# Kernel tuning notes

Hardware: AMD Instinct MI355X
Metric: run time of the kernel (lower is better)

Reference implementation:

```python
import jax, jax.numpy as jnp
import numpy as np

L, D = 6, 2048


def setup_inputs() -> dict:
    key = jax.random.key(0)
    ks = jax.random.split(key, 6)
    # 0.05 scale keeps repeated matrix compositions numerically tame
    W_upper = jax.random.normal(ks[0], (L, D, D), dtype=jnp.float32) * 0.05
    W_lower = jax.random.normal(ks[1], (L, D, D), dtype=jnp.float32) * 0.05
    b_upper = jax.random.normal(ks[2], (L, D), dtype=jnp.float32)
    b_lower = jax.random.normal(ks[3], (L, D), dtype=jnp.float32)
    ub = jax.random.normal(ks[4], (L, D), dtype=jnp.float32)
    lb = jax.random.normal(ks[5], (L, D), dtype=jnp.float32)
    return dict(W_upper=W_upper, W_lower=W_lower, b_upper=b_upper,
                b_lower=b_lower, ub=ub, lb=lb)


def _pos(W):
    # M * W  where M = (W >= 0)
    return jnp.where(W >= 0, W, jnp.zeros_like(W))


def _neg(W):
    # ~M * W where M = (W >= 0)
    return jnp.where(W >= 0, jnp.zeros_like(W), W)


def reference(W_upper, W_lower, b_upper, b_lower, ub, lb):
    # Layer index L-1 is `self`; backsubstitute toward layer 0 (input layer).
    Wu, Wl = W_upper[-1], W_lower[-1]          # [D, D]
    bu, bl = b_upper[-1], b_lower[-1]          # [D]
    best_ub, best_lb = ub[-1], lb[-1]          # [D]
    n_layers = W_upper.shape[0]
    for i in range(n_layers - 2, -1, -1):      # prev = layer i
        Wu_p, Wu_n = _pos(Wu), _neg(Wu)
        Wl_p, Wl_n = _pos(Wl), _neg(Wl)
        # concrete bounds through prev's pre-activation bounds
        cur_ub = Wu_p @ ub[i] + Wu_n @ lb[i] + bu
        cur_lb = Wl_p @ lb[i] + Wl_n @ ub[i] + bl
        best_ub = jnp.minimum(best_ub, cur_ub)
        best_lb = jnp.maximum(best_lb, cur_lb)
        # compose symbolic bounds with prev layer's relaxation
        bu = Wu_p @ b_upper[i] + Wu_n @ b_lower[i] + bu
        bl = Wl_p @ b_lower[i] + Wl_n @ b_upper[i] + bl
        Wu = Wu_p @ W_upper[i] + Wu_n @ W_lower[i]
        Wl = Wl_p @ W_lower[i] + Wl_n @ W_upper[i]
    # final concretization against the input layer's bounds (layer 0)
    Wu_p, Wu_n = _pos(Wu), _neg(Wu)
    Wl_p, Wl_n = _pos(Wl), _neg(Wl)
    cur_ub = Wu_p @ ub[0] + Wu_n @ lb[0] + bu
    cur_lb = Wl_p @ lb[0] + Wl_n @ ub[0] + bl
    best_ub = jnp.minimum(best_ub, cur_ub)
    best_lb = jnp.maximum(best_lb, cur_lb)
    return best_ub, best_lb
```

## Files before the change

kernel.cpp:

```cpp
#include <hip/hip_runtime.h>

#define D 2048
#define DD ((size_t)D * (size_t)D)

typedef __attribute__((ext_vector_type(8))) short bf16x8;
typedef __attribute__((ext_vector_type(16))) float f32x16;

#define GLOBAL_AS __attribute__((address_space(1)))
#define LDS_AS __attribute__((address_space(3)))

__device__ inline unsigned short f2bf(float f) {
  unsigned u = __float_as_uint(f);
  u += 0x7fffu + ((u >> 16) & 1u);
  return (unsigned short)(u >> 16);
}

__global__ void init_vecs(const float* __restrict__ b_upper5,
                          const float* __restrict__ b_lower5,
                          const float* __restrict__ ub5,
                          const float* __restrict__ lb5,
                          float* __restrict__ bu, float* __restrict__ bl,
                          float* __restrict__ out) {
  int t = blockIdx.x * blockDim.x + threadIdx.x;
  if (t < D) {
    bu[t] = b_upper5[t];
    bl[t] = b_lower5[t];
    out[t] = ub5[t];
    out[D + t] = lb5[t];
  }
}

__global__ __launch_bounds__(256) void prep(
    const float* __restrict__ Wu, const float* __restrict__ Wl,
    const float* __restrict__ ubi, const float* __restrict__ lbi,
    const float* __restrict__ bupi, const float* __restrict__ bloi,
    float* __restrict__ bu, float* __restrict__ bl,
    float* __restrict__ best,
    unsigned short* __restrict__ oU, unsigned short* __restrict__ oL,
    const float* __restrict__ Wup, const float* __restrict__ Wlo,
    unsigned short* __restrict__ BsT, unsigned short* __restrict__ BdT,
    int update_bias, int write16) {
  __shared__ float red[4][4];
  __shared__ unsigned short sS[64][68];
  __shared__ unsigned short sD[64][68];

  const int t = threadIdx.x;

  if (blockIdx.x < 2048) {
    const int r = blockIdx.x;
    const size_t base = (size_t)r * D + t * 8;
    const int c = t * 8;

    float4 wu0 = *(const float4*)(Wu + base), wu1 = *(const float4*)(Wu + base + 4);
    float4 wl0 = *(const float4*)(Wl + base), wl1 = *(const float4*)(Wl + base + 4);
    float4 u0 = *(const float4*)(ubi + c),  u1 = *(const float4*)(ubi + c + 4);
    float4 l0 = *(const float4*)(lbi + c),  l1 = *(const float4*)(lbi + c + 4);
    float4 p0 = *(const float4*)(bupi + c), p1 = *(const float4*)(bupi + c + 4);
    float4 n0 = *(const float4*)(bloi + c), n1 = *(const float4*)(bloi + c + 4);

    float wu[8] = {wu0.x, wu0.y, wu0.z, wu0.w, wu1.x, wu1.y, wu1.z, wu1.w};
    float wl[8] = {wl0.x, wl0.y, wl0.z, wl0.w, wl1.x, wl1.y, wl1.z, wl1.w};
    float uu[8] = {u0.x, u0.y, u0.z, u0.w, u1.x, u1.y, u1.z, u1.w};
    float ll[8] = {l0.x, l0.y, l0.z, l0.w, l1.x, l1.y, l1.z, l1.w};
    float pp[8] = {p0.x, p0.y, p0.z, p0.w, p1.x, p1.y, p1.z, p1.w};
    float nn[8] = {n0.x, n0.y, n0.z, n0.w, n1.x, n1.y, n1.z, n1.w};

    float su_c = 0.f, su_b = 0.f, sl_c = 0.f, sl_b = 0.f;
    #pragma unroll
    for (int j = 0; j < 8; ++j) {
      su_c += wu[j] * (wu[j] >= 0.f ? uu[j] : ll[j]);
      su_b += wu[j] * (wu[j] >= 0.f ? pp[j] : nn[j]);
      sl_c += wl[j] * (wl[j] >= 0.f ? ll[j] : uu[j]);
      sl_b += wl[j] * (wl[j] >= 0.f ? nn[j] : pp[j]);
    }

    if (write16) {
      uint4 w;
      w.x = f2bf(wu[0]) | ((unsigned)f2bf(wu[1]) << 16);
      w.y = f2bf(wu[2]) | ((unsigned)f2bf(wu[3]) << 16);
      w.z = f2bf(wu[4]) | ((unsigned)f2bf(wu[5]) << 16);
      w.w = f2bf(wu[6]) | ((unsigned)f2bf(wu[7]) << 16);
      *(uint4*)(oU + base) = w;
      w.x = f2bf(wl[0]) | ((unsigned)f2bf(wl[1]) << 16);
      w.y = f2bf(wl[2]) | ((unsigned)f2bf(wl[3]) << 16);
      w.z = f2bf(wl[4]) | ((unsigned)f2bf(wl[5]) << 16);
      w.w = f2bf(wl[6]) | ((unsigned)f2bf(wl[7]) << 16);
      *(uint4*)(oL + base) = w;
    }

    #pragma unroll
    for (int off = 32; off; off >>= 1) {
      su_c += __shfl_down(su_c, off);
      su_b += __shfl_down(su_b, off);
      sl_c += __shfl_down(sl_c, off);
      sl_b += __shfl_down(sl_b, off);
    }
    int wave = t >> 6;
    if ((t & 63) == 0) {
      red[0][wave] = su_c; red[1][wave] = su_b;
      red[2][wave] = sl_c; red[3][wave] = sl_b;
    }
    __syncthreads();
    if (t == 0) {
      float a = red[0][0] + red[0][1] + red[0][2] + red[0][3];
      float b = red[1][0] + red[1][1] + red[1][2] + red[1][3];
      float cc = red[2][0] + red[2][1] + red[2][2] + red[2][3];
      float d = red[3][0] + red[3][1] + red[3][2] + red[3][3];
      float bu_old = bu[r], bl_old = bl[r];
      best[r]     = fminf(best[r],     a + bu_old);
      best[D + r] = fmaxf(best[D + r], cc + bl_old);
      if (update_bias) {
        bu[r] = b + bu_old;
        bl[r] = d + bl_old;
      }
    }
  } else {
    const int bx = blockIdx.x - 2048;
    const int k0 = (bx >> 5) * 64, c0 = (bx & 31) * 64;
    const int tx = t & 15, ty = t >> 4;
    #pragma unroll
    for (int r = 0; r < 4; ++r) {
      int kk = ty + r * 16;
      size_t g = (size_t)(k0 + kk) * D + c0 + tx * 4;
      float4 up = *(const float4*)(Wup + g);
      float4 lo = *(const float4*)(Wlo + g);
      sS[kk][tx * 4 + 0] = f2bf((up.x + lo.x) * 0.5f);
      sS[kk][tx * 4 + 1] = f2bf((up.y + lo.y) * 0.5f);
      sS[kk][tx * 4 + 2] = f2bf((up.z + lo.z) * 0.5f);
      sS[kk][tx * 4 + 3] = f2bf((up.w + lo.w) * 0.5f);
      sD[kk][tx * 4 + 0] = f2bf((up.x - lo.x) * 0.5f);
      sD[kk][tx * 4 + 1] = f2bf((up.y - lo.y) * 0.5f);
      sD[kk][tx * 4 + 2] = f2bf((up.z - lo.z) * 0.5f);
      sD[kk][tx * 4 + 3] = f2bf((up.w - lo.w) * 0.5f);
    }
    __syncthreads();
    #pragma unroll
    for (int r = 0; r < 4; ++r) {
      int cc = ty + r * 16;
      int kq = tx * 4;
      unsigned a0 = sS[kq + 0][cc] | ((unsigned)sS[kq + 1][cc] << 16);
      unsigned a1 = sS[kq + 2][cc] | ((unsigned)sS[kq + 3][cc] << 16);
      *(uint2*)(BsT + (size_t)(c0 + cc) * D + k0 + kq) = make_uint2(a0, a1);
      a0 = sD[kq + 0][cc] | ((unsigned)sD[kq + 1][cc] << 16);
      a1 = sD[kq + 2][cc] | ((unsigned)sD[kq + 3][cc] << 16);
      *(uint2*)(BdT + (size_t)(c0 + cc) * D + k0 + kq) = make_uint2(a0, a1);
    }
  }
}

__global__ __launch_bounds__(512) void gemm_fused(
    const unsigned short* __restrict__ w16U,
    const unsigned short* __restrict__ w16L,
    const unsigned short* __restrict__ BsT,
    const unsigned short* __restrict__ BdT,
    float* __restrict__ Cu, float* __restrict__ Cl) {
  const int row0 = blockIdx.y * 128, col0 = blockIdx.x * 128;

  __shared__ unsigned char lds[65536];

  const int tid = threadIdx.x;
  const int lane = tid & 63, wid = tid >> 6;
  const int grp = wid >> 2;
  const int w2 = wid & 3;
  const int wr = w2 >> 1, wc = w2 & 1;
  const int l31 = lane & 31, kh = lane >> 5;

  const int srow = lane >> 2;
  const int soff = (lane & 3) * 16;
  const int row = wid * 16 + srow;
  const int sw = soff ^ (((row >> 1) & 3) << 4);

  const unsigned short* gAU = w16U + (size_t)(row0 + row) * D + (sw >> 1);
  const unsigned short* gAL = w16L + (size_t)(row0 + row) * D + (sw >> 1);
  const unsigned short* gBs = BsT + (size_t)(col0 + row) * D + (sw >> 1);
  const unsigned short* gBd = BdT + (size_t)(col0 + row) * D + (sw >> 1);

  f32x16 acc[2][2] = {};

  int aoff[2][2], boff[2][2];
  #pragma unroll
  for (int mb = 0; mb < 2; ++mb)
    #pragma unroll
    for (int ks = 0; ks < 2; ++ks) {
      int ar = wr * 64 + mb * 32 + l31;
      aoff[mb][ks] = ar * 64 + ((ks * 32 + kh * 16) ^ (((ar >> 1) & 3) << 4));
    }
  #pragma unroll
  for (int nb = 0; nb < 2; ++nb)
    #pragma unroll
    for (int ks = 0; ks < 2; ++ks) {
      int bc = wc * 64 + nb * 32 + l31;
      boff[nb][ks] = bc * 64 + ((ks * 32 + kh * 16) ^ (((bc >> 1) & 3) << 4));
    }

  #define STAGE(curb, kt)                                                          \
    do {                                                                           \
      unsigned dst = (unsigned)(curb) * 8192u + (unsigned)wid * 1024u;             \
      __builtin_amdgcn_global_load_lds((const GLOBAL_AS unsigned*)(gAU + (kt)),    \
          (LDS_AS unsigned*)(lds + 0 + dst), 16, 0, 0);                            \
      __builtin_amdgcn_global_load_lds((const GLOBAL_AS unsigned*)(gAL + (kt)),    \
          (LDS_AS unsigned*)(lds + 16384 + dst), 16, 0, 0);                        \
      __builtin_amdgcn_global_load_lds((const GLOBAL_AS unsigned*)(gBs + (kt)),    \
          (LDS_AS unsigned*)(lds + 32768 + dst), 16, 0, 0);                        \
      __builtin_amdgcn_global_load_lds((const GLOBAL_AS unsigned*)(gBd + (kt)),    \
          (LDS_AS unsigned*)(lds + 49152 + dst), 16, 0, 0);                        \
    } while (0)

  STAGE(0, 0);
  __syncthreads();

  int cur = 0;
  const unsigned Abase = grp ? 16384u : 0u;
  for (int t = 0; t < 64; ++t) {
    if (t < 63) STAGE(cur ^ 1, (t + 1) * 32);

    const unsigned char* Ab = lds + Abase + cur * 8192;
    const unsigned char* Sb = lds + 32768 + cur * 8192;
    const unsigned char* Db = lds + 49152 + cur * 8192;

    bf16x8 aw[2][2], av[2][2], bs[2][2], bd[2][2];
    #pragma unroll
    for (int mb = 0; mb < 2; ++mb)
      #pragma unroll
      for (int ks = 0; ks < 2; ++ks) {
        aw[mb][ks] = *(const bf16x8*)(Ab + aoff[mb][ks]);
        av[mb][ks] = aw[mb][ks] & (short)0x7fff;
      }
    #pragma unroll
    for (int nb = 0; nb < 2; ++nb)
      #pragma unroll
      for (int ks = 0; ks < 2; ++ks) {
        bs[nb][ks] = *(const bf16x8*)(Sb + boff[nb][ks]);
        bf16x8 d = *(const bf16x8*)(Db + boff[nb][ks]);
        if (grp) d ^= (short)0x8000;
        bd[nb][ks] = d;
      }

    #pragma unroll
    for (int mb = 0; mb < 2; ++mb)
      #pragma unroll
      for (int nb = 0; nb < 2; ++nb)
        #pragma unroll
        for (int ks = 0; ks < 2; ++ks) {
          acc[mb][nb] = __builtin_amdgcn_mfma_f32_32x32x16_bf16(
              aw[mb][ks], bs[nb][ks], acc[mb][nb], 0, 0, 0);
          acc[mb][nb] = __builtin_amdgcn_mfma_f32_32x32x16_bf16(
              av[mb][ks], bd[nb][ks], acc[mb][nb], 0, 0, 0);
        }

    __syncthreads();
    cur ^= 1;
  }
  #undef STAGE

  float* C = grp ? Cl : Cu;
  #pragma unroll
  for (int mb = 0; mb < 2; ++mb)
    #pragma unroll
    for (int nb = 0; nb < 2; ++nb) {
      const int colg = col0 + wc * 64 + nb * 32 + l31;
      const int rowb = row0 + wr * 64 + mb * 32 + kh * 4;
      #pragma unroll
      for (int g = 0; g < 4; ++g)
        #pragma unroll
        for (int j = 0; j < 4; ++j)
          C[(size_t)(rowb + g * 8 + j) * D + colg] = acc[mb][nb][g * 4 + j];
    }
}

extern "C" void kernel_launch(void* const* d_in, const int* in_sizes, int n_in,
                              void* d_out, int out_size, void* d_ws, size_t ws_size,
                              hipStream_t stream) {
  const float* W_upper = (const float*)d_in[0];
  const float* W_lower = (const float*)d_in[1];
  const float* b_upper = (const float*)d_in[2];
  const float* b_lower = (const float*)d_in[3];
  const float* ub      = (const float*)d_in[4];
  const float* lb      = (const float*)d_in[5];
  float* out = (float*)d_out;
  float* ws  = (float*)d_ws;

  float* curU = ws;
  float* curL = ws + DD;
  unsigned short* w16U = (unsigned short*)(ws + 2 * DD);
  unsigned short* w16L = w16U + DD;
  unsigned short* BsT  = w16L + DD;
  unsigned short* BdT  = BsT + DD;
  float* bu = (float*)(BdT + DD);
  float* bl = bu + D;

  init_vecs<<<(D + 255) / 256, 256, 0, stream>>>(
      b_upper + 5 * D, b_lower + 5 * D, ub + 5 * D, lb + 5 * D, bu, bl, out);

  const float* cU = W_upper + 5 * DD;
  const float* cL = W_lower + 5 * DD;
  for (int i = 4; i >= 0; --i) {
    prep<<<3072, 256, 0, stream>>>(cU, cL, ub + (size_t)i * D, lb + (size_t)i * D,
                                   b_upper + (size_t)i * D, b_lower + (size_t)i * D,
                                   bu, bl, out, w16U, w16L,
                                   W_upper + (size_t)i * DD, W_lower + (size_t)i * DD,
                                   BsT, BdT, 1, 1);
    gemm_fused<<<dim3(16, 16), 512, 0, stream>>>(w16U, w16L, BsT, BdT, curU, curL);
    cU = curU; cL = curL;
  }
  prep<<<2048, 256, 0, stream>>>(cU, cL, ub, lb, b_upper, b_lower,
                                 bu, bl, out, w16U, w16L,
                                 (const float*)nullptr, (const float*)nullptr,
                                 (unsigned short*)nullptr, (unsigned short*)nullptr,
                                 0, 0);
}
```

Baseline: 508.9 us.

## Double GEMM K-tile to 64, add XCD-aware block remap, use dynamic LDS

Raises the GEMM K-step from 32 to 64 using 128 KB of dynamic LDS (two 64 KB stages), so each block runs half as many loop iterations and barriers. The LDS swizzle moves to 128-byte rows with an 8-way XOR pattern. A 1D grid with a block-id remap sends contiguous runs of output tiles to each XCD to improve L2 reuse of the A rows. The trade-off is heavy LDS use, which allows only one block per CU, and a launch-bounds hint that may limit registers.

Result: faster. 460.1 us (-9.6%).

```diff
diff --git a/kernel.cpp b/kernel.cpp
--- a/kernel.cpp
+++ b/kernel.cpp
@@ -148,15 +148,17 @@
   }
 }
 
-__global__ __launch_bounds__(512) void gemm_fused(
+__global__ __launch_bounds__(512, 2) void gemm_fused(
     const unsigned short* __restrict__ w16U,
     const unsigned short* __restrict__ w16L,
     const unsigned short* __restrict__ BsT,
     const unsigned short* __restrict__ BdT,
     float* __restrict__ Cu, float* __restrict__ Cl) {
-  const int row0 = blockIdx.y * 128, col0 = blockIdx.x * 128;
-
-  __shared__ unsigned char lds[65536];
+  extern __shared__ unsigned char lds[];
+
+  const int bid = blockIdx.x;
+  const int vid = (bid & 7) * 32 + (bid >> 3);
+  const int row0 = (vid >> 4) * 128, col0 = (vid & 15) * 128;
 
   const int tid = threadIdx.x;
   const int lane = tid & 63, wid = tid >> 6;
@@ -165,45 +167,57 @@
   const int wr = w2 >> 1, wc = w2 & 1;
   const int l31 = lane & 31, kh = lane >> 5;
 
-  const int srow = lane >> 2;
-  const int soff = (lane & 3) * 16;
-  const int row = wid * 16 + srow;
-  const int sw = soff ^ (((row >> 1) & 3) << 4);
-
-  const unsigned short* gAU = w16U + (size_t)(row0 + row) * D + (sw >> 1);
-  const unsigned short* gAL = w16L + (size_t)(row0 + row) * D + (sw >> 1);
-  const unsigned short* gBs = BsT + (size_t)(col0 + row) * D + (sw >> 1);
-  const unsigned short* gBd = BdT + (size_t)(col0 + row) * D + (sw >> 1);
+  const int srow8 = lane >> 3;
+  const int slot  = lane & 7;
+  int rowc[2], swel[2];
+  #pragma unroll
+  for (int c = 0; c < 2; ++c) {
+    rowc[c] = (wid + c * 8) * 8 + srow8;
+    swel[c] = (slot ^ (rowc[c] & 7)) * 8;
+  }
+  const unsigned short* gAU[2]; const unsigned short* gAL[2];
+  const unsigned short* gBs[2]; const unsigned short* gBd[2];
+  #pragma unroll
+  for (int c = 0; c < 2; ++c) {
+    gAU[c] = w16U + (size_t)(row0 + rowc[c]) * D + swel[c];
+    gAL[c] = w16L + (size_t)(row0 + rowc[c]) * D + swel[c];
+    gBs[c] = BsT + (size_t)(col0 + rowc[c]) * D + swel[c];
+    gBd[c] = BdT + (size_t)(col0 + rowc[c]) * D + swel[c];
+  }
 
   f32x16 acc[2][2] = {};
 
-  int aoff[2][2], boff[2][2];
-  #pragma unroll
-  for (int mb = 0; mb < 2; ++mb)
-    #pragma unroll
-    for (int ks = 0; ks < 2; ++ks) {
-      int ar = wr * 64 + mb * 32 + l31;
-      aoff[mb][ks] = ar * 64 + ((ks * 32 + kh * 16) ^ (((ar >> 1) & 3) << 4));
-    }
-  #pragma unroll
-  for (int nb = 0; nb < 2; ++nb)
-    #pragma unroll
-    for (int ks = 0; ks < 2; ++ks) {
-      int bc = wc * 64 + nb * 32 + l31;
-      boff[nb][ks] = bc * 64 + ((ks * 32 + kh * 16) ^ (((bc >> 1) & 3) << 4));
-    }
+  int aoff[2][4], boff[2][4];
+  #pragma unroll
+  for (int mb = 0; mb < 2; ++mb) {
+    int ar = wr * 64 + mb * 32 + l31;
+    #pragma unroll
+    for (int ks = 0; ks < 4; ++ks)
+      aoff[mb][ks] = ar * 128 + (((ks * 2 + kh) ^ (ar & 7)) * 16);
+  }
+  #pragma unroll
+  for (int nb = 0; nb < 2; ++nb) {
+    int bc = wc * 64 + nb * 32 + l31;
+    #pragma unroll
+    for (int ks = 0; ks < 4; ++ks)
+      boff[nb][ks] = bc * 128 + (((ks * 2 + kh) ^ (bc & 7)) * 16);
+  }
 
   #define STAGE(curb, kt)                                                          \
     do {                                                                           \
-      unsigned dst = (unsigned)(curb) * 8192u + (unsigned)wid * 1024u;             \
-      __builtin_amdgcn_global_load_lds((const GLOBAL_AS unsigned*)(gAU + (kt)),    \
-          (LDS_AS unsigned*)(lds + 0 + dst), 16, 0, 0);                            \
-      __builtin_amdgcn_global_load_lds((const GLOBAL_AS unsigned*)(gAL + (kt)),    \
-          (LDS_AS unsigned*)(lds + 16384 + dst), 16, 0, 0);                        \
-      __builtin_amdgcn_global_load_lds((const GLOBAL_AS unsigned*)(gBs + (kt)),    \
-          (LDS_AS unsigned*)(lds + 32768 + dst), 16, 0, 0);                        \
-      __builtin_amdgcn_global_load_lds((const GLOBAL_AS unsigned*)(gBd + (kt)),    \
-          (LDS_AS unsigned*)(lds + 49152 + dst), 16, 0, 0);                        \
+      unsigned bb = (unsigned)(curb) * 65536u;                                     \
+      _Pragma("unroll")                                                            \
+      for (int c = 0; c < 2; ++c) {                                                \
+        unsigned dst = bb + (unsigned)(wid + c * 8) * 1024u;                       \
+        __builtin_amdgcn_global_load_lds((const GLOBAL_AS unsigned*)(gAU[c] + (kt)),\
+            (LDS_AS unsigned*)(lds + 0 + dst), 16, 0, 0);                          \
+        __builtin_amdgcn_global_load_lds((const GLOBAL_AS unsigned*)(gAL[c] + (kt)),\
+            (LDS_AS unsigned*)(lds + 16384 + dst), 16, 0, 0);                      \
+        __builtin_amdgcn_global_load_lds((const GLOBAL_AS unsigned*)(gBs[c] + (kt)),\
+            (LDS_AS unsigned*)(lds + 32768 + dst), 16, 0, 0);                      \
+        __builtin_amdgcn_global_load_lds((const GLOBAL_AS unsigned*)(gBd[c] + (kt)),\
+            (LDS_AS unsigned*)(lds + 49152 + dst), 16, 0, 0);                      \
+      }                                                                            \
     } while (0)
 
   STAGE(0, 0);
@@ -211,42 +225,34 @@
 
   int cur = 0;
   const unsigned Abase = grp ? 16384u : 0u;
-  for (int t = 0; t < 64; ++t) {
-    if (t < 63) STAGE(cur ^ 1, (t + 1) * 32);
-
-    const unsigned char* Ab = lds + Abase + cur * 8192;
-    const unsigned char* Sb = lds + 32768 + cur * 8192;
-    const unsigned char* Db = lds + 49152 + cur * 8192;
-
-    bf16x8 aw[2][2], av[2][2], bs[2][2], bd[2][2];
-    #pragma unroll
-    for (int mb = 0; mb < 2; ++mb)
-      #pragma unroll
-      for (int ks = 0; ks < 2; ++ks) {
-        aw[mb][ks] = *(const bf16x8*)(Ab + aoff[mb][ks]);
-        av[mb][ks] = aw[mb][ks] & (short)0x7fff;
-      }
-    #pragma unroll
-    for (int nb = 0; nb < 2; ++nb)
-      #pragma unroll
-      for (int ks = 0; ks < 2; ++ks) {
-        bs[nb][ks] = *(const bf16x8*)(Sb + boff[nb][ks]);
-        bf16x8 d = *(const bf16x8*)(Db + boff[nb][ks]);
-        if (grp) d ^= (short)0x8000;
-        bd[nb][ks] = d;
-      }
-
-    #pragma unroll
-    for (int mb = 0; mb < 2; ++mb)
-      #pragma unroll
-      for (int nb = 0; nb < 2; ++nb)
-        #pragma unroll
-        for (int ks = 0; ks < 2; ++ks) {
-          acc[mb][nb] = __builtin_amdgcn_mfma_f32_32x32x16_bf16(
-              aw[mb][ks], bs[nb][ks], acc[mb][nb], 0, 0, 0);
-          acc[mb][nb] = __builtin_amdgcn_mfma_f32_32x32x16_bf16(
-              av[mb][ks], bd[nb][ks], acc[mb][nb], 0, 0, 0);
-        }
+  for (int t = 0; t < 32; ++t) {
+    if (t < 31) STAGE(cur ^ 1, (t + 1) * 64);
+
+    const unsigned char* Ab = lds + Abase + cur * 65536;
+    const unsigned char* Sb = lds + 32768 + cur * 65536;
+    const unsigned char* Db = lds + 49152 + cur * 65536;
+
+    #pragma unroll
+    for (int ks = 0; ks < 4; ++ks) {
+      bf16x8 aw0 = *(const bf16x8*)(Ab + aoff[0][ks]);
+      bf16x8 aw1 = *(const bf16x8*)(Ab + aoff[1][ks]);
+      bf16x8 bs0 = *(const bf16x8*)(Sb + boff[0][ks]);
+      bf16x8 bs1 = *(const bf16x8*)(Sb + boff[1][ks]);
+      bf16x8 bd0 = *(const bf16x8*)(Db + boff[0][ks]);
+      bf16x8 bd1 = *(const bf16x8*)(Db + boff[1][ks]);
+      if (grp) { bd0 ^= (short)0x8000; bd1 ^= (short)0x8000; }
+      bf16x8 av0 = aw0 & (short)0x7fff;
+      bf16x8 av1 = aw1 & (short)0x7fff;
+
+      acc[0][0] = __builtin_amdgcn_mfma_f32_32x32x16_bf16(aw0, bs0, acc[0][0], 0, 0, 0);
+      acc[0][0] = __builtin_amdgcn_mfma_f32_32x32x16_bf16(av0, bd0, acc[0][0], 0, 0, 0);
+      acc[0][1] = __builtin_amdgcn_mfma_f32_32x32x16_bf16(aw0, bs1, acc[0][1], 0, 0, 0);
+      acc[0][1] = __builtin_amdgcn_mfma_f32_32x32x16_bf16(av0, bd1, acc[0][1], 0, 0, 0);
+      acc[1][0] = __builtin_amdgcn_mfma_f32_32x32x16_bf16(aw1, bs0, acc[1][0], 0, 0, 0);
+      acc[1][0] = __builtin_amdgcn_mfma_f32_32x32x16_bf16(av1, bd0, acc[1][0], 0, 0, 0);
+      acc[1][1] = __builtin_amdgcn_mfma_f32_32x32x16_bf16(aw1, bs1, acc[1][1], 0, 0, 0);
+      acc[1][1] = __builtin_amdgcn_mfma_f32_32x32x16_bf16(av1, bd1, acc[1][1], 0, 0, 0);
+    }
 
     __syncthreads();
     cur ^= 1;
@@ -289,6 +295,9 @@
   float* bu = (float*)(BdT + DD);
   float* bl = bu + D;
 
+  static_cast<void>(hipFuncSetAttribute(
+      (const void*)gemm_fused, hipFuncAttributeMaxDynamicSharedMemorySize, 131072));
+
   init_vecs<<<(D + 255) / 256, 256, 0, stream>>>(
       b_upper + 5 * D, b_lower + 5 * D, ub + 5 * D, lb + 5 * D, bu, bl, out);
 
@@ -300,7 +309,7 @@
                                    bu, bl, out, w16U, w16L,
                                    W_upper + (size_t)i * DD, W_lower + (size_t)i * DD,
                                    BsT, BdT, 1, 1);
-    gemm_fused<<<dim3(16, 16), 512, 0, stream>>>(w16U, w16L, BsT, BdT, curU, curL);
+    gemm_fused<<<256, 512, 131072, stream>>>(w16U, w16L, BsT, BdT, curU, curL);
     cU = curU; cL = curL;
   }
   prep<<<2048, 256, 0, stream>>>(cU, cL, ub, lb, b_upper, b_lower,
```
